# Performance work log

Measured on AMD Instinct MI355X. Metric: run time of the kernel, lower is better.

The kernel has to match this reference:

```python
import jax, jax.numpy as jnp
import numpy as np

N_STATES = 16          # 2**memory_length, memory_length hard-coded to 4 in the source
MEM = 4                # memory_length
T = 16384              # transmission_length
B = 256                # batch size


def setup_inputs() -> dict:
    key = jax.random.key(0)
    k1, k2 = jax.random.split(key)
    # received channel observations, one scalar per time step per batch element
    y = jax.random.normal(k1, (B, T + MEM), dtype=jnp.float32)
    # ISI channel taps (exponentially decaying, COST-channel style)
    h = jnp.exp(-0.7 * jnp.arange(MEM, dtype=jnp.float32))
    return {"y": y, "h": h}


def reference(y, h):
    n = N_STATES
    states = jnp.arange(n)
    # bit k of state s is the transmitted bit x_{t-k} (newest bit at LSB, since
    # next = (2*s + b) mod n under create_transition_table's packbits layout)
    bits = ((states[:, None] >> jnp.arange(MEM)[None, :]) & 1).astype(jnp.float32)  # [16,4]
    symbols = 1.0 - 2.0 * bits                     # BPSKModulator.modulate: 1 - 2c
    expected = symbols @ h                          # [16] expected channel output per state
    # predecessors of state ns: table[ns, j] = (ns >> 1) + j * n/2  (matches packbits table)
    pred_table = (states[:, None] >> 1) + jnp.array([0, 1])[None, :] * (n // 2)  # [16,2]

    def acs(in_prob, y_t):
        # add-compare-select over the 2 predecessors of each state
        cand = in_prob[:, pred_table]                              # [B,16,2]
        j = jnp.argmin(cand, axis=2)                               # [B,16] survivor index
        cost = (y_t[:, None] - expected[None, :]) ** 2             # [B,16] branch metric
        out_prob = jnp.min(cand, axis=2) + cost                    # [B,16]
        prev = pred_table[states[None, :], j]                      # [B,16] survivor predecessor
        return out_prob, prev.astype(jnp.int32)

    in0 = jnp.zeros((y.shape[0], n), dtype=y.dtype)                # initial_in_prob
    _, prev_states = jax.lax.scan(acs, in0, y.T)                   # prev_states: [T+MEM, B, 16]

    # traceback from start_state = 0
    def tb(state, prev_t):
        new_state = jnp.take_along_axis(prev_t, state[:, None], axis=1)[:, 0]  # [B]
        bit = (new_state >= n // 2).astype(jnp.float32)
        return new_state, bit

    start = jnp.zeros((y.shape[0],), dtype=jnp.int32)
    _, bits_rev = jax.lax.scan(tb, start, prev_states, reverse=True)  # [T+MEM, B], time order
    ml_path_bits = bits_rev.T                                         # [B, T+MEM]
    return ml_path_bits[:, :T]                                        # drop last memory_length bits
```

## Files before the change

### kernel.cpp

```cpp
#include <hip/hip_runtime.h>


#define DEV static __device__ __forceinline__

static constexpr int T_OUT = 16384;
static constexpr int TT    = 16388;
static constexpr int BB    = 256;
static constexpr int CHUNK = 64;
static constexpr int NFULL = 256;
static constexpr int NC    = 257;
static constexpr int CROW  = 68;

static constexpr unsigned long long IPI_TAB[4] = {
  0x4b5a6978c3d2e1f0ULL,
  0x4cb35da26e917f80ULL,
  0x46ceb93157dfa820ULL,
  0x4567cdefba983210ULL,
};

DEV int pi_of(int phi, int l){
  int l0=l&1, l1=(l>>1)&1, l2=(l>>2)&1, l3=(l>>3)&1;
  switch(phi & 3){
    case 0:  return (l2)      | ((l2^l0)<<1) | ((l2^l1)<<2) | ((l3^l2)<<3);
    case 1:  return (l3^l2)   | ((l2)<<1)    | ((l2^l0)<<2) | ((l2^l1)<<3);
    case 2:  return (l2^l1)   | ((l3^l2)<<1) | ((l2)<<2)    | ((l2^l0)<<3);
    default: return (l2^l0)   | ((l2^l1)<<1) | ((l3^l2)<<2) | ((l2)<<3);
  }
}

template<int CTRL>
DEV float dppmov(float x){
  return __int_as_float(__builtin_amdgcn_update_dpp(0, __float_as_int(x), CTRL, 0xF, 0xF, true));
}

template<int PH>
DEV float partner_of(float p){
  if constexpr (PH == 0) return dppmov<0x128>(p);
  else if constexpr (PH == 1) return dppmov<0x4E>(p);
  else if constexpr (PH == 2) return dppmov<0xB1>(p);
  else return dppmov<0x140>(p);
}

DEV float exp_of_state(int s, float h0, float h1, float h2, float h3){
  float e =            ((s     ) & 1) ? -h0 : h0;
  e = __fadd_rn(e, (((s >> 1)) & 1) ? -h1 : h1);
  e = __fadd_rn(e, (((s >> 2)) & 1) ? -h2 : h2);
  e = __fadd_rn(e, (((s >> 3)) & 1) ? -h3 : h3);
  return e;
}

DEV void chain8(float& p, float m0, float m1, float m2, float m3,
                float m4, float m5, float m6, float m7){
  float mn;
  asm volatile(
    "v_min_f32_dpp %1, %0, %0 row_ror:8 row_mask:0xf bank_mask:0xf\n\t"
    "v_add_f32 %0, %1, %2\n\t"
    "s_nop 1\n\t"
    "v_min_f32_dpp %1, %0, %0 quad_perm:[2,3,0,1] row_mask:0xf bank_mask:0xf\n\t"
    "v_add_f32 %0, %1, %3\n\t"
    "s_nop 1\n\t"
    "v_min_f32_dpp %1, %0, %0 quad_perm:[1,0,3,2] row_mask:0xf bank_mask:0xf\n\t"
    "v_add_f32 %0, %1, %4\n\t"
    "s_nop 1\n\t"
    "v_min_f32_dpp %1, %0, %0 row_mirror row_mask:0xf bank_mask:0xf\n\t"
    "v_add_f32 %0, %1, %5\n\t"
    "s_nop 1\n\t"
    "v_min_f32_dpp %1, %0, %0 row_ror:8 row_mask:0xf bank_mask:0xf\n\t"
    "v_add_f32 %0, %1, %6\n\t"
    "s_nop 1\n\t"
    "v_min_f32_dpp %1, %0, %0 quad_perm:[2,3,0,1] row_mask:0xf bank_mask:0xf\n\t"
    "v_add_f32 %0, %1, %7\n\t"
    "s_nop 1\n\t"
    "v_min_f32_dpp %1, %0, %0 quad_perm:[1,0,3,2] row_mask:0xf bank_mask:0xf\n\t"
    "v_add_f32 %0, %1, %8\n\t"
    "s_nop 1\n\t"
    "v_min_f32_dpp %1, %0, %0 row_mirror row_mask:0xf bank_mask:0xf\n\t"
    "v_add_f32 %0, %1, %9"
    : "+v"(p), "=&v"(mn)
    : "v"(m0), "v"(m1), "v"(m2), "v"(m3),
      "v"(m4), "v"(m5), "v"(m6), "v"(m7));
}

DEV void gload_lds16(const float* g, float* l){
  __builtin_amdgcn_global_load_lds(
      (const __attribute__((address_space(1))) void*)(g),
      (__attribute__((address_space(3))) void*)(l), 16, 0, 0);
}

DEV void wg_barrier(){
  asm volatile("s_waitcnt lgkmcnt(0)" ::: "memory");
  __builtin_amdgcn_s_barrier();
}

__global__ __launch_bounds__(192, 1) void k_forward(const float* __restrict__ y,
                                                    const float* __restrict__ h,
                                                    float* __restrict__ ckpt){
  __shared__ float ring[8][256];
  __shared__ float cost[2][64 * CROW];
  __shared__ float cks[64 * 64];

  const int tid  = threadIdx.x;
  const int wv   = tid >> 6;
  const int lane = tid & 63;

  if (wv == 0){
    const int l16 = lane & 15, s4 = lane >> 4;
    const int st0 = pi_of(0, l16);
    const int row = l16 * 4 + s4;

    float4 cqA[16], cqB[16];
    float p = 0.0f;

    wg_barrier();
    wg_barrier();
    {
      const float* cb = &cost[0][0];
      #pragma unroll
      for (int g = 0; g < 16; ++g)
        cqA[g] = *(const float4*)(cb + row * CROW + 4 * g);
    }
    wg_barrier();

    for (int k = 0; k < NFULL; k += 2){
      {
        const float* cb = &cost[1][0];
        #pragma unroll
        for (int g = 0; g < 16; ++g)
          cqB[g] = *(const float4*)(cb + row * CROW + 4 * g);
        __builtin_amdgcn_sched_barrier(0);
        #pragma unroll
        for (int g = 0; g < 16; g += 2)
          chain8(p, cqA[g].x, cqA[g].y, cqA[g].z, cqA[g].w,
                    cqA[g+1].x, cqA[g+1].y, cqA[g+1].z, cqA[g+1].w);
        cks[(k & 63) * 64 + s4 * 16 + st0] = p;
      }
      wg_barrier();
      {
        const float* cb = &cost[0][0];
        #pragma unroll
        for (int g = 0; g < 16; ++g)
          cqA[g] = *(const float4*)(cb + row * CROW + 4 * g);
        __builtin_amdgcn_sched_barrier(0);
        #pragma unroll
        for (int g = 0; g < 16; g += 2)
          chain8(p, cqB[g].x, cqB[g].y, cqB[g].z, cqB[g].w,
                    cqB[g+1].x, cqB[g+1].y, cqB[g+1].z, cqB[g+1].w);
        cks[((k + 1) & 63) * 64 + s4 * 16 + st0] = p;
        if (((k + 1) & 63) == 63){
          const int seg = (k + 1) >> 6;
          #pragma unroll 8
          for (int ch = 0; ch < 64; ++ch){
            const size_t chunkIdx = (size_t)seg * 64 + ch;
            ckpt[(chunkIdx * BB + blockIdx.x * 4) * 16 + lane] = cks[ch * 64 + lane];
          }
          asm volatile("s_waitcnt vmcnt(0)" ::: "memory");
        }
      }
      wg_barrier();
    }
  } else {
    const int gbase = (wv - 1) * 8;
    const int pl16  = lane >> 2;
    const int ps4   = lane & 3;
    const float h0 = h[0], h1 = h[1], h2 = h[2], h3 = h[3];
    const float EA = exp_of_state(pi_of(1,pl16), h0,h1,h2,h3);
    const float EB = exp_of_state(pi_of(2,pl16), h0,h1,h2,h3);
    const float EC = exp_of_state(pi_of(3,pl16), h0,h1,h2,h3);
    const float ED = exp_of_state(pi_of(0,pl16), h0,h1,h2,h3);
    const float* ysrc = y + (size_t)(blockIdx.x * 4 + ps4) * TT + pl16 * 4;

    #define PRODUCE(RB, CB)                                                   \
      {                                                                       \
        const float* rb = (RB);                                               \
        float* cb = (CB);                                                     \
        _Pragma("unroll")                                                     \
        for (int g2 = 0; g2 < 8; ++g2){                                       \
          const int g = gbase + g2;                                           \
          float4 yv = *(const float4*)(rb + g * 16 + ps4 * 4);                \
          float4 c; float d;                                                  \
          d = __fsub_rn(yv.x, EA); c.x = __fmul_rn(d, d);                     \
          d = __fsub_rn(yv.y, EB); c.y = __fmul_rn(d, d);                     \
          d = __fsub_rn(yv.z, EC); c.z = __fmul_rn(d, d);                     \
          d = __fsub_rn(yv.w, ED); c.w = __fmul_rn(d, d);                     \
          *(float4*)(cb + lane * CROW + 4 * g) = c;                           \
        }                                                                     \
      }

    if (wv == 1){
      #pragma unroll
      for (int q = 0; q < 8; ++q)
        gload_lds16(ysrc + q * CHUNK, &ring[q][0]);
      asm volatile("s_waitcnt vmcnt(6)" ::: "memory");
    }
    wg_barrier();
    PRODUCE(&ring[0][0], &cost[0][0]);
    wg_barrier();
    PRODUCE(&ring[1][0], &cost[1][0]);
    if (wv == 1){
      gload_lds16(ysrc + 8 * CHUNK, &ring[0][0]);
      asm volatile("s_waitcnt vmcnt(6)" ::: "memory");
    }
    wg_barrier();

    for (int k = 0; k < NFULL; k += 2){
      if (k + 2 < NFULL) PRODUCE(&ring[(k + 2) & 7][0], &cost[0][0]);
      if (wv == 1){
        const int ci = (k + 9 < NFULL) ? k + 9 : NFULL - 1;
        gload_lds16(ysrc + ci * CHUNK, &ring[(k + 9) & 7][0]);
        asm volatile("s_waitcnt vmcnt(6)" ::: "memory");
      }
      wg_barrier();
      if (k + 3 < NFULL) PRODUCE(&ring[(k + 3) & 7][0], &cost[1][0]);
      if (wv == 1){
        const int ci = (k + 10 < NFULL) ? k + 10 : NFULL - 1;
        gload_lds16(ysrc + ci * CHUNK, &ring[(k + 10) & 7][0]);
        asm volatile("s_waitcnt vmcnt(6)" ::: "memory");
      }
      wg_barrier();
    }
    #undef PRODUCE
  }
}

template<int PH>
DEV unsigned rstep(float& p, float yv, float E, bool role){
  float partner = partner_of<PH>(p);
  float c1 = role ? p : partner;
  float c0 = role ? partner : p;
  unsigned d = (c1 < c0) ? 1u : 0u;
  float mn = fminf(p, partner);
  float dd = __fsub_rn(yv, E);
  p = __fadd_rn(mn, __fmul_rn(dd, dd));
  return d;
}

__global__ __launch_bounds__(256) void k_replay(const float* __restrict__ y,
                                                const float* __restrict__ h,
                                                const float* __restrict__ ckpt,
                                                unsigned long long* __restrict__ bits,
                                                unsigned char* __restrict__ map){
  const int gt   = blockIdx.x * 256 + threadIdx.x;
  const int pair = gt >> 4;
  const int l16  = gt & 15;
  const int c    = pair >> 8;
  const int seq  = pair & 255;
  const float h0 = h[0], h1 = h[1], h2 = h[2], h3 = h[3];
  const float EA = exp_of_state(pi_of(1,l16), h0,h1,h2,h3);
  const float EB = exp_of_state(pi_of(2,l16), h0,h1,h2,h3);
  const float EC = exp_of_state(pi_of(3,l16), h0,h1,h2,h3);
  const float ED = exp_of_state(pi_of(0,l16), h0,h1,h2,h3);
  const bool r0 = (((l16>>3) ^ (l16>>2)) & 1) != 0;
  const bool r1 = (((l16>>2) ^ (l16>>1)) & 1) != 0;
  const bool r2 = (((l16>>2) ^  l16    ) & 1) != 0;
  const bool r3 = (( l16>>2)             & 1) != 0;
  const int  st0 = pi_of(0, l16);

  float p = (c == 0) ? 0.0f : ckpt[((size_t)(c - 1) * BB + seq) * 16 + st0];
  const float* yc = y + (size_t)seq * TT + c * CHUNK;
  unsigned lo = 0, hi = 0;

  if (c < NFULL){
    #pragma unroll
    for (int g = 0; g < 16; ++g){
      float4 yv = *(const float4*)(yc + 4*g);
      unsigned d0 = rstep<0>(p, yv.x, EA, r0);
      unsigned d1 = rstep<1>(p, yv.y, EB, r1);
      unsigned d2 = rstep<2>(p, yv.z, EC, r2);
      unsigned d3 = rstep<3>(p, yv.w, ED, r3);
      const int t = 4 * g;
      if (t < 32) lo |= (d0 << t) | (d1 << (t+1)) | (d2 << (t+2)) | (d3 << (t+3));
      else        hi |= (d0 << (t-32)) | (d1 << (t-31)) | (d2 << (t-30)) | (d3 << (t-29));
    }
  } else {
    float4 yv = *(const float4*)(yc);
    unsigned d0 = rstep<0>(p, yv.x, EA, r0);
    unsigned d1 = rstep<1>(p, yv.y, EB, r1);
    unsigned d2 = rstep<2>(p, yv.z, EC, r2);
    unsigned d3 = rstep<3>(p, yv.w, ED, r3);
    lo = d0 | (d1 << 1) | (d2 << 2) | (d3 << 3);
  }

  const int base = (threadIdx.x & 63) & 48;
  int s = l16;
  unsigned long long pb = 0ull;
  if (c < NFULL){
    #pragma unroll
    for (int j = 63; j >= 0; --j){
      int l = (int)((IPI_TAB[(j + 1) & 3] >> (4 * s)) & 15);
      unsigned hw = __shfl((j >= 32) ? hi : lo, base + l);
      unsigned long long b = (hw >> (j & 31)) & 1;
      s = (s >> 1) | ((int)b << 3);
      pb |= b << j;
    }
  } else {
    #pragma unroll
    for (int j = 3; j >= 0; --j){
      int l = (int)((IPI_TAB[(j + 1) & 3] >> (4 * s)) & 15);
      unsigned hw = __shfl(lo, base + l);
      unsigned long long b = (hw >> j) & 1;
      s = (s >> 1) | ((int)b << 3);
      pb |= b << j;
    }
  }
  bits[(size_t)pair * 16 + l16] = pb;
  map [(size_t)pair * 16 + l16] = (unsigned char)s;
}

__global__ __launch_bounds__(256) void k_compose(const unsigned char* __restrict__ map,
                                                 unsigned char* __restrict__ Earr){
  const int seq = threadIdx.x;
  int s = 0;
  Earr[(size_t)NFULL * BB + seq] = 0;
  #pragma unroll 4
  for (int c = NC - 1; c >= 1; --c){
    const uint4 mr = *(const uint4*)(map + ((size_t)c * BB + seq) * 16);
    unsigned wsel = (s < 8) ? ((s < 4) ? mr.x : mr.y) : ((s < 12) ? mr.z : mr.w);
    s = (wsel >> ((s & 3) * 8)) & 15;
    Earr[(size_t)(c - 1) * BB + seq] = (unsigned char)s;
  }
}

__global__ __launch_bounds__(256) void k_emit(const unsigned long long* __restrict__ bits,
                                              const unsigned char* __restrict__ Earr,
                                              float* __restrict__ out){
  const int gt   = blockIdx.x * 256 + threadIdx.x;
  const int pair = gt >> 4;
  const int l16  = gt & 15;
  const int c    = pair >> 8;
  const int seq  = pair & 255;
  const int e    = Earr[(size_t)c * BB + seq];
  const unsigned long long w = bits[(size_t)pair * 16 + e];
  const int j0 = l16 * 4;
  float4 f;
  f.x = (float)((w >> (j0    )) & 1);
  f.y = (float)((w >> (j0 + 1)) & 1);
  f.z = (float)((w >> (j0 + 2)) & 1);
  f.w = (float)((w >> (j0 + 3)) & 1);
  *(float4*)(out + (size_t)seq * T_OUT + c * CHUNK + j0) = f;
}

extern "C" void kernel_launch(void* const* d_in, const int* in_sizes, int n_in,
                              void* d_out, int out_size, void* d_ws, size_t ws_size,
                              hipStream_t stream){
  const float* y = (const float*)d_in[0];
  const float* h = (const float*)d_in[1];
  float* out = (float*)d_out;

  const size_t CKPT_B = (size_t)NFULL * BB * 16 * 4;
  const size_t BITS_B = (size_t)NC * BB * 16 * 8;
  const size_t MAP_B  = (size_t)NC * BB * 16;
  const size_t E_B    = (size_t)NC * BB;
  if (ws_size < CKPT_B + BITS_B + MAP_B + E_B) return;

  char* ws = (char*)d_ws;
  float*              ckpt = (float*)ws;
  unsigned long long* bits = (unsigned long long*)(ws + CKPT_B);
  unsigned char*      map  = (unsigned char*)(ws + CKPT_B + BITS_B);
  unsigned char*      Earr = (unsigned char*)(ws + CKPT_B + BITS_B + MAP_B);

  hipLaunchKernelGGL(k_forward, dim3(64),   dim3(192), 0, stream, y, h, ckpt);
  hipLaunchKernelGGL(k_replay,  dim3(4112), dim3(256), 0, stream, y, h, ckpt, bits, map);
  hipLaunchKernelGGL(k_compose, dim3(1),    dim3(256), 0, stream, map, Earr);
  hipLaunchKernelGGL(k_emit,    dim3(4096), dim3(256), 0, stream, bits, Earr, out);
}
```

Baseline: 288.6 us.

## Interleave two independent Viterbi chains per consumer wave to hide DPP latency

The forward checkpoint kernel now gives each consumer wave two independent groups of 4 sequences (8 per block), interleaving their DPP min/add chains so one chain's instructions fill the other's dependency stalls instead of s_nop padding. The block grows to 5 waves (two producer pairs) and the grid halves to 32 blocks, with doubled LDS ring, cost and checkpoint buffers. Using fewer blocks lowers CU-level parallelism and raises register pressure from four float4[16] arrays. The compose kernel's unroll factor also rises from 4 to 8.

```diff
diff --git a/kernel.cpp b/kernel.cpp
--- a/kernel.cpp
+++ b/kernel.cpp
@@ -49,36 +49,28 @@
   return e;
 }
 
-DEV void chain8(float& p, float m0, float m1, float m2, float m3,
-                float m4, float m5, float m6, float m7){
-  float mn;
+DEV void chain4x2(float& pA, float& pB, const float4 mA, const float4 mB){
+  float tA, tB;
   asm volatile(
-    "v_min_f32_dpp %1, %0, %0 row_ror:8 row_mask:0xf bank_mask:0xf\n\t"
-    "v_add_f32 %0, %1, %2\n\t"
-    "s_nop 1\n\t"
-    "v_min_f32_dpp %1, %0, %0 quad_perm:[2,3,0,1] row_mask:0xf bank_mask:0xf\n\t"
-    "v_add_f32 %0, %1, %3\n\t"
-    "s_nop 1\n\t"
-    "v_min_f32_dpp %1, %0, %0 quad_perm:[1,0,3,2] row_mask:0xf bank_mask:0xf\n\t"
-    "v_add_f32 %0, %1, %4\n\t"
-    "s_nop 1\n\t"
-    "v_min_f32_dpp %1, %0, %0 row_mirror row_mask:0xf bank_mask:0xf\n\t"
-    "v_add_f32 %0, %1, %5\n\t"
-    "s_nop 1\n\t"
-    "v_min_f32_dpp %1, %0, %0 row_ror:8 row_mask:0xf bank_mask:0xf\n\t"
-    "v_add_f32 %0, %1, %6\n\t"
-    "s_nop 1\n\t"
-    "v_min_f32_dpp %1, %0, %0 quad_perm:[2,3,0,1] row_mask:0xf bank_mask:0xf\n\t"
-    "v_add_f32 %0, %1, %7\n\t"
-    "s_nop 1\n\t"
-    "v_min_f32_dpp %1, %0, %0 quad_perm:[1,0,3,2] row_mask:0xf bank_mask:0xf\n\t"
-    "v_add_f32 %0, %1, %8\n\t"
-    "s_nop 1\n\t"
-    "v_min_f32_dpp %1, %0, %0 row_mirror row_mask:0xf bank_mask:0xf\n\t"
-    "v_add_f32 %0, %1, %9"
-    : "+v"(p), "=&v"(mn)
-    : "v"(m0), "v"(m1), "v"(m2), "v"(m3),
-      "v"(m4), "v"(m5), "v"(m6), "v"(m7));
+    "v_min_f32_dpp %2, %0, %0 row_ror:8 row_mask:0xf bank_mask:0xf\n\t"
+    "v_min_f32_dpp %3, %1, %1 row_ror:8 row_mask:0xf bank_mask:0xf\n\t"
+    "v_add_f32 %0, %2, %4\n\t"
+    "v_add_f32 %1, %3, %8\n\t"
+    "v_min_f32_dpp %2, %0, %0 quad_perm:[2,3,0,1] row_mask:0xf bank_mask:0xf\n\t"
+    "v_min_f32_dpp %3, %1, %1 quad_perm:[2,3,0,1] row_mask:0xf bank_mask:0xf\n\t"
+    "v_add_f32 %0, %2, %5\n\t"
+    "v_add_f32 %1, %3, %9\n\t"
+    "v_min_f32_dpp %2, %0, %0 quad_perm:[1,0,3,2] row_mask:0xf bank_mask:0xf\n\t"
+    "v_min_f32_dpp %3, %1, %1 quad_perm:[1,0,3,2] row_mask:0xf bank_mask:0xf\n\t"
+    "v_add_f32 %0, %2, %6\n\t"
+    "v_add_f32 %1, %3, %10\n\t"
+    "v_min_f32_dpp %2, %0, %0 row_mirror row_mask:0xf bank_mask:0xf\n\t"
+    "v_min_f32_dpp %3, %1, %1 row_mirror row_mask:0xf bank_mask:0xf\n\t"
+    "v_add_f32 %0, %2, %7\n\t"
+    "v_add_f32 %1, %3, %11"
+    : "+v"(pA), "+v"(pB), "=&v"(tA), "=&v"(tB)
+    : "v"(mA.x), "v"(mA.y), "v"(mA.z), "v"(mA.w),
+      "v"(mB.x), "v"(mB.y), "v"(mB.z), "v"(mB.w));
 }
 
 DEV void gload_lds16(const float* g, float* l){
@@ -92,12 +84,14 @@
   __builtin_amdgcn_s_barrier();
 }
 
-__global__ __launch_bounds__(192, 1) void k_forward(const float* __restrict__ y,
+__global__ __launch_bounds__(320, 1) void k_forward(const float* __restrict__ y,
                                                     const float* __restrict__ h,
                                                     float* __restrict__ ckpt){
-  __shared__ float ring[8][256];
-  __shared__ float cost[2][64 * CROW];
-  __shared__ float cks[64 * 64];
+  __shared__ float ringA[8][256];
+  __shared__ float ringB[8][256];
+  __shared__ float costA[2][64 * CROW];
+  __shared__ float costB[2][64 * CROW];
+  __shared__ float cks[64 * 128];
 
   const int tid  = threadIdx.x;
   const int wv   = tid >> 6;
@@ -108,50 +102,58 @@
     const int st0 = pi_of(0, l16);
     const int row = l16 * 4 + s4;
 
-    float4 cqA[16], cqB[16];
-    float p = 0.0f;
+    float4 qa[16], qb[16], ra[16], rb[16];
+    float pA = 0.0f, pB = 0.0f;
 
     wg_barrier();
     wg_barrier();
     {
-      const float* cb = &cost[0][0];
+      const float* ca = &costA[0][0];
+      const float* cb = &costB[0][0];
       #pragma unroll
-      for (int g = 0; g < 16; ++g)
-        cqA[g] = *(const float4*)(cb + row * CROW + 4 * g);
+      for (int g = 0; g < 16; ++g) qa[g] = *(const float4*)(ca + row * CROW + 4 * g);
+      #pragma unroll
+      for (int g = 0; g < 16; ++g) qb[g] = *(const float4*)(cb + row * CROW + 4 * g);
     }
     wg_barrier();
 
     for (int k = 0; k < NFULL; k += 2){
       {
-        const float* cb = &cost[1][0];
+        const float* ca = &costA[1][0];
+        const float* cb = &costB[1][0];
+        #pragma unroll
+        for (int g = 0; g < 16; ++g) ra[g] = *(const float4*)(ca + row * CROW + 4 * g);
+        #pragma unroll
+        for (int g = 0; g < 16; ++g) rb[g] = *(const float4*)(cb + row * CROW + 4 * g);
+        __builtin_amdgcn_sched_barrier(0);
         #pragma unroll
         for (int g = 0; g < 16; ++g)
-          cqB[g] = *(const float4*)(cb + row * CROW + 4 * g);
-        __builtin_amdgcn_sched_barrier(0);
-        #pragma unroll
-        for (int g = 0; g < 16; g += 2)
-          chain8(p, cqA[g].x, cqA[g].y, cqA[g].z, cqA[g].w,
-                    cqA[g+1].x, cqA[g+1].y, cqA[g+1].z, cqA[g+1].w);
-        cks[(k & 63) * 64 + s4 * 16 + st0] = p;
+          chain4x2(pA, pB, qa[g], qb[g]);
+        cks[(k & 63) * 128 +      s4 * 16 + st0] = pA;
+        cks[(k & 63) * 128 + 64 + s4 * 16 + st0] = pB;
       }
       wg_barrier();
       {
-        const float* cb = &cost[0][0];
+        const float* ca = &costA[0][0];
+        const float* cb = &costB[0][0];
+        #pragma unroll
+        for (int g = 0; g < 16; ++g) qa[g] = *(const float4*)(ca + row * CROW + 4 * g);
+        #pragma unroll
+        for (int g = 0; g < 16; ++g) qb[g] = *(const float4*)(cb + row * CROW + 4 * g);
+        __builtin_amdgcn_sched_barrier(0);
         #pragma unroll
         for (int g = 0; g < 16; ++g)
-          cqA[g] = *(const float4*)(cb + row * CROW + 4 * g);
-        __builtin_amdgcn_sched_barrier(0);
-        #pragma unroll
-        for (int g = 0; g < 16; g += 2)
-          chain8(p, cqB[g].x, cqB[g].y, cqB[g].z, cqB[g].w,
-                    cqB[g+1].x, cqB[g+1].y, cqB[g+1].z, cqB[g+1].w);
-        cks[((k + 1) & 63) * 64 + s4 * 16 + st0] = p;
+          chain4x2(pA, pB, ra[g], rb[g]);
+        cks[((k + 1) & 63) * 128 +      s4 * 16 + st0] = pA;
+        cks[((k + 1) & 63) * 128 + 64 + s4 * 16 + st0] = pB;
         if (((k + 1) & 63) == 63){
           const int seg = (k + 1) >> 6;
           #pragma unroll 8
           for (int ch = 0; ch < 64; ++ch){
             const size_t chunkIdx = (size_t)seg * 64 + ch;
-            ckpt[(chunkIdx * BB + blockIdx.x * 4) * 16 + lane] = cks[ch * 64 + lane];
+            float* dst = ckpt + (chunkIdx * BB + blockIdx.x * 8) * 16;
+            dst[lane]      = cks[ch * 128 + lane];
+            dst[64 + lane] = cks[ch * 128 + 64 + lane];
           }
           asm volatile("s_waitcnt vmcnt(0)" ::: "memory");
         }
@@ -159,61 +161,69 @@
       wg_barrier();
     }
   } else {
-    const int gbase = (wv - 1) * 8;
-    const int pl16  = lane >> 2;
-    const int ps4   = lane & 3;
+    const bool isA   = (wv <= 2);
+    const int  pw    = isA ? (wv - 1) : (wv - 3);
+    const int  gbase = pw * 8;
+    float* ring0 = isA ? &ringA[0][0] : &ringB[0][0];
+    float* cost0 = isA ? &costA[0][0] : &costB[0][0];
+    float* cost1 = isA ? &costA[1][0] : &costB[1][0];
+    const bool stager = (pw == 0);
+
+    const int pl16 = lane >> 2;
+    const int ps4  = lane & 3;
     const float h0 = h[0], h1 = h[1], h2 = h[2], h3 = h[3];
     const float EA = exp_of_state(pi_of(1,pl16), h0,h1,h2,h3);
     const float EB = exp_of_state(pi_of(2,pl16), h0,h1,h2,h3);
     const float EC = exp_of_state(pi_of(3,pl16), h0,h1,h2,h3);
     const float ED = exp_of_state(pi_of(0,pl16), h0,h1,h2,h3);
-    const float* ysrc = y + (size_t)(blockIdx.x * 4 + ps4) * TT + pl16 * 4;
+    const float* ysrc = y + (size_t)(blockIdx.x * 8 + (isA ? 0 : 4) + ps4) * TT
+                          + pl16 * 4;
 
     #define PRODUCE(RB, CB)                                                   \
       {                                                                       \
-        const float* rb = (RB);                                               \
-        float* cb = (CB);                                                     \
+        const float* rb_ = (RB);                                              \
+        float* cb_ = (CB);                                                    \
         _Pragma("unroll")                                                     \
         for (int g2 = 0; g2 < 8; ++g2){                                       \
           const int g = gbase + g2;                                           \
-          float4 yv = *(const float4*)(rb + g * 16 + ps4 * 4);                \
+          float4 yv = *(const float4*)(rb_ + g * 16 + ps4 * 4);               \
           float4 c; float d;                                                  \
           d = __fsub_rn(yv.x, EA); c.x = __fmul_rn(d, d);                     \
           d = __fsub_rn(yv.y, EB); c.y = __fmul_rn(d, d);                     \
           d = __fsub_rn(yv.z, EC); c.z = __fmul_rn(d, d);                     \
           d = __fsub_rn(yv.w, ED); c.w = __fmul_rn(d, d);                     \
-          *(float4*)(cb + lane * CROW + 4 * g) = c;                           \
+          *(float4*)(cb_ + lane * CROW + 4 * g) = c;                          \
         }                                                                     \
       }
 
-    if (wv == 1){
+    if (stager){
       #pragma unroll
       for (int q = 0; q < 8; ++q)
-        gload_lds16(ysrc + q * CHUNK, &ring[q][0]);
+        gload_lds16(ysrc + q * CHUNK, ring0 + q * 256);
       asm volatile("s_waitcnt vmcnt(6)" ::: "memory");
     }
     wg_barrier();
-    PRODUCE(&ring[0][0], &cost[0][0]);
-    wg_barrier();
-    PRODUCE(&ring[1][0], &cost[1][0]);
-    if (wv == 1){
-      gload_lds16(ysrc + 8 * CHUNK, &ring[0][0]);
+    PRODUCE(ring0 + 0 * 256, cost0);
+    wg_barrier();
+    PRODUCE(ring0 + 1 * 256, cost1);
+    if (stager){
+      gload_lds16(ysrc + 8 * CHUNK, ring0 + 0 * 256);
       asm volatile("s_waitcnt vmcnt(6)" ::: "memory");
     }
     wg_barrier();
 
     for (int k = 0; k < NFULL; k += 2){
-      if (k + 2 < NFULL) PRODUCE(&ring[(k + 2) & 7][0], &cost[0][0]);
-      if (wv == 1){
+      if (k + 2 < NFULL) PRODUCE(ring0 + ((k + 2) & 7) * 256, cost0);
+      if (stager){
         const int ci = (k + 9 < NFULL) ? k + 9 : NFULL - 1;
-        gload_lds16(ysrc + ci * CHUNK, &ring[(k + 9) & 7][0]);
+        gload_lds16(ysrc + ci * CHUNK, ring0 + ((k + 9) & 7) * 256);
         asm volatile("s_waitcnt vmcnt(6)" ::: "memory");
       }
       wg_barrier();
-      if (k + 3 < NFULL) PRODUCE(&ring[(k + 3) & 7][0], &cost[1][0]);
-      if (wv == 1){
+      if (k + 3 < NFULL) PRODUCE(ring0 + ((k + 3) & 7) * 256, cost1);
+      if (stager){
         const int ci = (k + 10 < NFULL) ? k + 10 : NFULL - 1;
-        gload_lds16(ysrc + ci * CHUNK, &ring[(k + 10) & 7][0]);
+        gload_lds16(ysrc + ci * CHUNK, ring0 + ((k + 10) & 7) * 256);
         asm volatile("s_waitcnt vmcnt(6)" ::: "memory");
       }
       wg_barrier();
@@ -311,7 +321,7 @@
   const int seq = threadIdx.x;
   int s = 0;
   Earr[(size_t)NFULL * BB + seq] = 0;
-  #pragma unroll 4
+  #pragma unroll 8
   for (int c = NC - 1; c >= 1; --c){
     const uint4 mr = *(const uint4*)(map + ((size_t)c * BB + seq) * 16);
     unsigned wsel = (s < 8) ? ((s < 4) ? mr.x : mr.y) : ((s < 12) ? mr.z : mr.w);
@@ -358,7 +368,7 @@
   unsigned char*      map  = (unsigned char*)(ws + CKPT_B + BITS_B);
   unsigned char*      Earr = (unsigned char*)(ws + CKPT_B + BITS_B + MAP_B);
 
-  hipLaunchKernelGGL(k_forward, dim3(64),   dim3(192), 0, stream, y, h, ckpt);
+  hipLaunchKernelGGL(k_forward, dim3(32),   dim3(320), 0, stream, y, h, ckpt);
   hipLaunchKernelGGL(k_replay,  dim3(4112), dim3(256), 0, stream, y, h, ckpt, bits, map);
   hipLaunchKernelGGL(k_compose, dim3(1),    dim3(256), 0, stream, map, Earr);
   hipLaunchKernelGGL(k_emit,    dim3(4096), dim3(256), 0, stream, bits, Earr, out);
```

Measured after the change: 388.3 us. +34.6%, slower.

## Fuse forward and replay kernels with counter-based producer-consumer overlap

Applied to the files above, without the earlier changes.

Merges the forward checkpoint kernel and the replay kernel into one persistent launch. 64 blocks run the forward recursion and publish checkpoints every 16 chunks with release counters, while 448 replay blocks spin on those counters and start replaying chunks as soon as their segment is ready. The aim is to overlap replay with the serial forward pass and drop a kernel launch boundary. In exchange it adds spin-wait polling and atomic traffic, and it relies on all blocks being co-resident to avoid deadlock. It also adds a tiny counter-zeroing kernel and raises the compose loop unroll.

```diff
diff --git a/kernel.cpp b/kernel.cpp
--- a/kernel.cpp
+++ b/kernel.cpp
@@ -10,6 +10,10 @@
 static constexpr int NFULL = 256;
 static constexpr int NC    = 257;
 static constexpr int CROW  = 68;
+static constexpr int FWD_BLOCKS = 64;
+static constexpr int RPL_BLOCKS = 448;
+static constexpr int NTILES = 4112;
+static constexpr int NSEG   = 16;
 
 static constexpr unsigned long long IPI_TAB[4] = {
   0x4b5a6978c3d2e1f0ULL,
@@ -88,138 +92,7 @@
 }
 
 DEV void wg_barrier(){
-  asm volatile("s_waitcnt lgkmcnt(0)" ::: "memory");
-  __builtin_amdgcn_s_barrier();
-}
-
-__global__ __launch_bounds__(192, 1) void k_forward(const float* __restrict__ y,
-                                                    const float* __restrict__ h,
-                                                    float* __restrict__ ckpt){
-  __shared__ float ring[8][256];
-  __shared__ float cost[2][64 * CROW];
-  __shared__ float cks[64 * 64];
-
-  const int tid  = threadIdx.x;
-  const int wv   = tid >> 6;
-  const int lane = tid & 63;
-
-  if (wv == 0){
-    const int l16 = lane & 15, s4 = lane >> 4;
-    const int st0 = pi_of(0, l16);
-    const int row = l16 * 4 + s4;
-
-    float4 cqA[16], cqB[16];
-    float p = 0.0f;
-
-    wg_barrier();
-    wg_barrier();
-    {
-      const float* cb = &cost[0][0];
-      #pragma unroll
-      for (int g = 0; g < 16; ++g)
-        cqA[g] = *(const float4*)(cb + row * CROW + 4 * g);
-    }
-    wg_barrier();
-
-    for (int k = 0; k < NFULL; k += 2){
-      {
-        const float* cb = &cost[1][0];
-        #pragma unroll
-        for (int g = 0; g < 16; ++g)
-          cqB[g] = *(const float4*)(cb + row * CROW + 4 * g);
-        __builtin_amdgcn_sched_barrier(0);
-        #pragma unroll
-        for (int g = 0; g < 16; g += 2)
-          chain8(p, cqA[g].x, cqA[g].y, cqA[g].z, cqA[g].w,
-                    cqA[g+1].x, cqA[g+1].y, cqA[g+1].z, cqA[g+1].w);
-        cks[(k & 63) * 64 + s4 * 16 + st0] = p;
-      }
-      wg_barrier();
-      {
-        const float* cb = &cost[0][0];
-        #pragma unroll
-        for (int g = 0; g < 16; ++g)
-          cqA[g] = *(const float4*)(cb + row * CROW + 4 * g);
-        __builtin_amdgcn_sched_barrier(0);
-        #pragma unroll
-        for (int g = 0; g < 16; g += 2)
-          chain8(p, cqB[g].x, cqB[g].y, cqB[g].z, cqB[g].w,
-                    cqB[g+1].x, cqB[g+1].y, cqB[g+1].z, cqB[g+1].w);
-        cks[((k + 1) & 63) * 64 + s4 * 16 + st0] = p;
-        if (((k + 1) & 63) == 63){
-          const int seg = (k + 1) >> 6;
-          #pragma unroll 8
-          for (int ch = 0; ch < 64; ++ch){
-            const size_t chunkIdx = (size_t)seg * 64 + ch;
-            ckpt[(chunkIdx * BB + blockIdx.x * 4) * 16 + lane] = cks[ch * 64 + lane];
-          }
-          asm volatile("s_waitcnt vmcnt(0)" ::: "memory");
-        }
-      }
-      wg_barrier();
-    }
-  } else {
-    const int gbase = (wv - 1) * 8;
-    const int pl16  = lane >> 2;
-    const int ps4   = lane & 3;
-    const float h0 = h[0], h1 = h[1], h2 = h[2], h3 = h[3];
-    const float EA = exp_of_state(pi_of(1,pl16), h0,h1,h2,h3);
-    const float EB = exp_of_state(pi_of(2,pl16), h0,h1,h2,h3);
-    const float EC = exp_of_state(pi_of(3,pl16), h0,h1,h2,h3);
-    const float ED = exp_of_state(pi_of(0,pl16), h0,h1,h2,h3);
-    const float* ysrc = y + (size_t)(blockIdx.x * 4 + ps4) * TT + pl16 * 4;
-
-    #define PRODUCE(RB, CB)                                                   \
-      {                                                                       \
-        const float* rb = (RB);                                               \
-        float* cb = (CB);                                                     \
-        _Pragma("unroll")                                                     \
-        for (int g2 = 0; g2 < 8; ++g2){                                       \
-          const int g = gbase + g2;                                           \
-          float4 yv = *(const float4*)(rb + g * 16 + ps4 * 4);                \
-          float4 c; float d;                                                  \
-          d = __fsub_rn(yv.x, EA); c.x = __fmul_rn(d, d);                     \
-          d = __fsub_rn(yv.y, EB); c.y = __fmul_rn(d, d);                     \
-          d = __fsub_rn(yv.z, EC); c.z = __fmul_rn(d, d);                     \
-          d = __fsub_rn(yv.w, ED); c.w = __fmul_rn(d, d);                     \
-          *(float4*)(cb + lane * CROW + 4 * g) = c;                           \
-        }                                                                     \
-      }
-
-    if (wv == 1){
-      #pragma unroll
-      for (int q = 0; q < 8; ++q)
-        gload_lds16(ysrc + q * CHUNK, &ring[q][0]);
-      asm volatile("s_waitcnt vmcnt(6)" ::: "memory");
-    }
-    wg_barrier();
-    PRODUCE(&ring[0][0], &cost[0][0]);
-    wg_barrier();
-    PRODUCE(&ring[1][0], &cost[1][0]);
-    if (wv == 1){
-      gload_lds16(ysrc + 8 * CHUNK, &ring[0][0]);
-      asm volatile("s_waitcnt vmcnt(6)" ::: "memory");
-    }
-    wg_barrier();
-
-    for (int k = 0; k < NFULL; k += 2){
-      if (k + 2 < NFULL) PRODUCE(&ring[(k + 2) & 7][0], &cost[0][0]);
-      if (wv == 1){
-        const int ci = (k + 9 < NFULL) ? k + 9 : NFULL - 1;
-        gload_lds16(ysrc + ci * CHUNK, &ring[(k + 9) & 7][0]);
-        asm volatile("s_waitcnt vmcnt(6)" ::: "memory");
-      }
-      wg_barrier();
-      if (k + 3 < NFULL) PRODUCE(&ring[(k + 3) & 7][0], &cost[1][0]);
-      if (wv == 1){
-        const int ci = (k + 10 < NFULL) ? k + 10 : NFULL - 1;
-        gload_lds16(ysrc + ci * CHUNK, &ring[(k + 10) & 7][0]);
-        asm volatile("s_waitcnt vmcnt(6)" ::: "memory");
-      }
-      wg_barrier();
-    }
-    #undef PRODUCE
-  }
+  asm volatile("s_waitcnt lgkmcnt(0)\n\ts_barrier" ::: "memory");
 }
 
 template<int PH>
@@ -234,76 +107,234 @@
   return d;
 }
 
-__global__ __launch_bounds__(256) void k_replay(const float* __restrict__ y,
-                                                const float* __restrict__ h,
-                                                const float* __restrict__ ckpt,
-                                                unsigned long long* __restrict__ bits,
-                                                unsigned char* __restrict__ map){
-  const int gt   = blockIdx.x * 256 + threadIdx.x;
-  const int pair = gt >> 4;
-  const int l16  = gt & 15;
-  const int c    = pair >> 8;
-  const int seq  = pair & 255;
-  const float h0 = h[0], h1 = h[1], h2 = h[2], h3 = h[3];
-  const float EA = exp_of_state(pi_of(1,l16), h0,h1,h2,h3);
-  const float EB = exp_of_state(pi_of(2,l16), h0,h1,h2,h3);
-  const float EC = exp_of_state(pi_of(3,l16), h0,h1,h2,h3);
-  const float ED = exp_of_state(pi_of(0,l16), h0,h1,h2,h3);
-  const bool r0 = (((l16>>3) ^ (l16>>2)) & 1) != 0;
-  const bool r1 = (((l16>>2) ^ (l16>>1)) & 1) != 0;
-  const bool r2 = (((l16>>2) ^  l16    ) & 1) != 0;
-  const bool r3 = (( l16>>2)             & 1) != 0;
-  const int  st0 = pi_of(0, l16);
-
-  float p = (c == 0) ? 0.0f : ckpt[((size_t)(c - 1) * BB + seq) * 16 + st0];
-  const float* yc = y + (size_t)seq * TT + c * CHUNK;
-  unsigned lo = 0, hi = 0;
-
-  if (c < NFULL){
-    #pragma unroll
-    for (int g = 0; g < 16; ++g){
-      float4 yv = *(const float4*)(yc + 4*g);
-      unsigned d0 = rstep<0>(p, yv.x, EA, r0);
-      unsigned d1 = rstep<1>(p, yv.y, EB, r1);
-      unsigned d2 = rstep<2>(p, yv.z, EC, r2);
-      unsigned d3 = rstep<3>(p, yv.w, ED, r3);
-      const int t = 4 * g;
-      if (t < 32) lo |= (d0 << t) | (d1 << (t+1)) | (d2 << (t+2)) | (d3 << (t+3));
-      else        hi |= (d0 << (t-32)) | (d1 << (t-31)) | (d2 << (t-30)) | (d3 << (t-29));
+__global__ void k_zero(unsigned* __restrict__ c){
+  for (int i = 0; i < NSEG; ++i) c[i] = 0u;
+}
+
+__global__ __launch_bounds__(256, 1) void k_main(const float* __restrict__ y,
+                                                 const float* __restrict__ h,
+                                                 float* __restrict__ ckpt,
+                                                 unsigned long long* __restrict__ bits,
+                                                 unsigned char* __restrict__ map,
+                                                 unsigned* __restrict__ counter){
+  __shared__ float ring[8][256];
+  __shared__ float costb[2][64 * CROW];
+  __shared__ float cks[16 * 64];
+
+  const int tid  = threadIdx.x;
+  const int lane = tid & 63;
+
+  if (blockIdx.x < FWD_BLOCKS){
+    const int wv  = tid >> 6;
+    const int blk = blockIdx.x;
+
+    if (wv == 0){
+      const int l16 = lane & 15, s4 = lane >> 4;
+      const int st0 = pi_of(0, l16);
+      const int row = l16 * 4 + s4;
+      float4 qA[16], qB[16];
+      float p = 0.0f;
+
+      wg_barrier();
+      wg_barrier();
+      {
+        const float* cb = &costb[0][0];
+        #pragma unroll
+        for (int g = 0; g < 16; ++g)
+          qA[g] = *(const float4*)(cb + row * CROW + 4 * g);
+      }
+      wg_barrier();
+
+      #define FLUSH(SEG)                                                      \
+        {                                                                     \
+          const int seg_ = (SEG);                                             \
+          _Pragma("unroll")                                                   \
+          for (int ch = 0; ch < 16; ++ch){                                    \
+            const size_t chunkIdx = (size_t)seg_ * 16 + ch;                   \
+            __hip_atomic_store(&ckpt[(chunkIdx * BB + blk * 4) * 16 + lane],  \
+                               cks[ch * 64 + lane],                           \
+                               __ATOMIC_RELAXED, __HIP_MEMORY_SCOPE_AGENT);   \
+          }                                                                   \
+          asm volatile("s_waitcnt vmcnt(0)" ::: "memory");                    \
+          if (lane == 0)                                                      \
+            __hip_atomic_fetch_add(&counter[seg_], 1u,                        \
+                                   __ATOMIC_RELEASE, __HIP_MEMORY_SCOPE_AGENT);\
+        }
+
+      for (int k = 0; k < NFULL; k += 2){
+        {
+          const float* cb = &costb[1][0];
+          #pragma unroll
+          for (int g = 0; g < 16; ++g)
+            qB[g] = *(const float4*)(cb + row * CROW + 4 * g);
+          __builtin_amdgcn_sched_barrier(0);
+          #pragma unroll
+          for (int g = 0; g < 16; g += 2)
+            chain8(p, qA[g].x, qA[g].y, qA[g].z, qA[g].w,
+                      qA[g+1].x, qA[g+1].y, qA[g+1].z, qA[g+1].w);
+          cks[(k & 15) * 64 + s4 * 16 + st0] = p;
+          wg_barrier();
+        }
+        {
+          const float* cb = &costb[0][0];
+          #pragma unroll
+          for (int g = 0; g < 16; ++g)
+            qA[g] = *(const float4*)(cb + row * CROW + 4 * g);
+          __builtin_amdgcn_sched_barrier(0);
+          #pragma unroll
+          for (int g = 0; g < 16; g += 2)
+            chain8(p, qB[g].x, qB[g].y, qB[g].z, qB[g].w,
+                      qB[g+1].x, qB[g+1].y, qB[g+1].z, qB[g+1].w);
+          cks[((k + 1) & 15) * 64 + s4 * 16 + st0] = p;
+          if (((k + 1) & 15) == 15) FLUSH((k + 1) >> 4);
+          wg_barrier();
+        }
+      }
+      #undef FLUSH
+    } else if (wv <= 2){
+      const int gbase = (wv - 1) * 8;
+      const int pl16  = lane >> 2;
+      const int ps4   = lane & 3;
+      const float h0 = h[0], h1 = h[1], h2 = h[2], h3 = h[3];
+      const float EA = exp_of_state(pi_of(1, pl16), h0, h1, h2, h3);
+      const float EB = exp_of_state(pi_of(2, pl16), h0, h1, h2, h3);
+      const float EC = exp_of_state(pi_of(3, pl16), h0, h1, h2, h3);
+      const float ED = exp_of_state(pi_of(0, pl16), h0, h1, h2, h3);
+      const float* ysrc = y + (size_t)(blk * 4 + ps4) * TT + pl16 * 4;
+
+      #define PRODUCE(RB, CB)                                                 \
+        {                                                                     \
+          const float* rb_ = (RB);                                            \
+          float* cb_ = (CB);                                                  \
+          _Pragma("unroll")                                                   \
+          for (int g2 = 0; g2 < 8; ++g2){                                     \
+            const int g = gbase + g2;                                         \
+            float4 yv = *(const float4*)(rb_ + g * 16 + ps4 * 4);             \
+            float4 c; float d_;                                               \
+            d_ = __fsub_rn(yv.x, EA); c.x = __fmul_rn(d_, d_);                \
+            d_ = __fsub_rn(yv.y, EB); c.y = __fmul_rn(d_, d_);                \
+            d_ = __fsub_rn(yv.z, EC); c.z = __fmul_rn(d_, d_);                \
+            d_ = __fsub_rn(yv.w, ED); c.w = __fmul_rn(d_, d_);                \
+            *(float4*)(cb_ + lane * CROW + 4 * g) = c;                        \
+          }                                                                   \
+        }
+
+      if (wv == 1){
+        #pragma unroll
+        for (int q = 0; q < 8; ++q)
+          gload_lds16(ysrc + q * CHUNK, &ring[q][0]);
+        asm volatile("s_waitcnt vmcnt(6)" ::: "memory");
+      }
+      wg_barrier();
+      PRODUCE(&ring[0][0], &costb[0][0]);
+      wg_barrier();
+      PRODUCE(&ring[1][0], &costb[1][0]);
+      if (wv == 1){
+        gload_lds16(ysrc + 8 * CHUNK, &ring[0][0]);
+        asm volatile("s_waitcnt vmcnt(6)" ::: "memory");
+      }
+      wg_barrier();
+
+      for (int k = 0; k < NFULL; k += 2){
+        if (k + 2 < NFULL) PRODUCE(&ring[(k + 2) & 7][0], &costb[0][0]);
+        if (wv == 1){
+          const int ci = (k + 9 < NFULL) ? k + 9 : NFULL - 1;
+          gload_lds16(ysrc + ci * CHUNK, &ring[(k + 9) & 7][0]);
+          asm volatile("s_waitcnt vmcnt(6)" ::: "memory");
+        }
+        wg_barrier();
+        if (k + 3 < NFULL) PRODUCE(&ring[(k + 3) & 7][0], &costb[1][0]);
+        if (wv == 1){
+          const int ci = (k + 10 < NFULL) ? k + 10 : NFULL - 1;
+          gload_lds16(ysrc + ci * CHUNK, &ring[(k + 10) & 7][0]);
+          asm volatile("s_waitcnt vmcnt(6)" ::: "memory");
+        }
+        wg_barrier();
+      }
+      #undef PRODUCE
+    } else {
+      for (int i = 0; i < 259; ++i) wg_barrier();
     }
   } else {
-    float4 yv = *(const float4*)(yc);
-    unsigned d0 = rstep<0>(p, yv.x, EA, r0);
-    unsigned d1 = rstep<1>(p, yv.y, EB, r1);
-    unsigned d2 = rstep<2>(p, yv.z, EC, r2);
-    unsigned d3 = rstep<3>(p, yv.w, ED, r3);
-    lo = d0 | (d1 << 1) | (d2 << 2) | (d3 << 3);
-  }
-
-  const int base = (threadIdx.x & 63) & 48;
-  int s = l16;
-  unsigned long long pb = 0ull;
-  if (c < NFULL){
-    #pragma unroll
-    for (int j = 63; j >= 0; --j){
-      int l = (int)((IPI_TAB[(j + 1) & 3] >> (4 * s)) & 15);
-      unsigned hw = __shfl((j >= 32) ? hi : lo, base + l);
-      unsigned long long b = (hw >> (j & 31)) & 1;
-      s = (s >> 1) | ((int)b << 3);
-      pb |= b << j;
-    }
-  } else {
-    #pragma unroll
-    for (int j = 3; j >= 0; --j){
-      int l = (int)((IPI_TAB[(j + 1) & 3] >> (4 * s)) & 15);
-      unsigned hw = __shfl(lo, base + l);
-      unsigned long long b = (hw >> j) & 1;
-      s = (s >> 1) | ((int)b << 3);
-      pb |= b << j;
+    const int rb  = blockIdx.x - FWD_BLOCKS;
+    const int l16 = tid & 15;
+    const int sub = tid >> 4;
+    const float h0 = h[0], h1 = h[1], h2 = h[2], h3 = h[3];
+    const float EA = exp_of_state(pi_of(1,l16), h0,h1,h2,h3);
+    const float EB = exp_of_state(pi_of(2,l16), h0,h1,h2,h3);
+    const float EC = exp_of_state(pi_of(3,l16), h0,h1,h2,h3);
+    const float ED = exp_of_state(pi_of(0,l16), h0,h1,h2,h3);
+    const bool r0 = (((l16>>3) ^ (l16>>2)) & 1) != 0;
+    const bool r1 = (((l16>>2) ^ (l16>>1)) & 1) != 0;
+    const bool r2 = (((l16>>2) ^  l16    ) & 1) != 0;
+    const bool r3 = (( l16>>2)             & 1) != 0;
+    const int  st0  = pi_of(0, l16);
+    const int  base = lane & 48;
+
+    for (int t = rb; t < NTILES; t += RPL_BLOCKS){
+      const int pair = t * 16 + sub;
+      const int c    = pair >> 8;
+      const int seq  = pair & 255;
+
+      if (c > 0){
+        const int seg = (c - 1) >> 4;
+        while (__hip_atomic_load(&counter[seg], __ATOMIC_ACQUIRE,
+                                 __HIP_MEMORY_SCOPE_AGENT) < (unsigned)FWD_BLOCKS)
+          __builtin_amdgcn_s_sleep(8);
+      }
+
+      float p = (c == 0) ? 0.0f
+        : __hip_atomic_load(&ckpt[((size_t)(c - 1) * BB + seq) * 16 + st0],
+                            __ATOMIC_RELAXED, __HIP_MEMORY_SCOPE_AGENT);
+      const float* yc = y + (size_t)seq * TT + c * CHUNK;
+      unsigned lo = 0, hi = 0;
+
+      if (c < NFULL){
+        #pragma unroll
+        for (int g = 0; g < 16; ++g){
+          float4 yv = *(const float4*)(yc + 4*g);
+          unsigned d0 = rstep<0>(p, yv.x, EA, r0);
+          unsigned d1 = rstep<1>(p, yv.y, EB, r1);
+          unsigned d2 = rstep<2>(p, yv.z, EC, r2);
+          unsigned d3 = rstep<3>(p, yv.w, ED, r3);
+          const int tt = 4 * g;
+          if (tt < 32) lo |= (d0 << tt) | (d1 << (tt+1)) | (d2 << (tt+2)) | (d3 << (tt+3));
+          else         hi |= (d0 << (tt-32)) | (d1 << (tt-31)) | (d2 << (tt-30)) | (d3 << (tt-29));
+        }
+      } else {
+        float4 yv = *(const float4*)(yc);
+        unsigned d0 = rstep<0>(p, yv.x, EA, r0);
+        unsigned d1 = rstep<1>(p, yv.y, EB, r1);
+        unsigned d2 = rstep<2>(p, yv.z, EC, r2);
+        unsigned d3 = rstep<3>(p, yv.w, ED, r3);
+        lo = d0 | (d1 << 1) | (d2 << 2) | (d3 << 3);
+      }
+
+      int s = l16;
+      unsigned long long pb = 0ull;
+      if (c < NFULL){
+        #pragma unroll
+        for (int j = 63; j >= 0; --j){
+          int l = (int)((IPI_TAB[(j + 1) & 3] >> (4 * s)) & 15);
+          unsigned hw = __shfl((j >= 32) ? hi : lo, base + l);
+          unsigned long long b = (hw >> (j & 31)) & 1;
+          s = (s >> 1) | ((int)b << 3);
+          pb |= b << j;
+        }
+      } else {
+        #pragma unroll
+        for (int j = 3; j >= 0; --j){
+          int l = (int)((IPI_TAB[(j + 1) & 3] >> (4 * s)) & 15);
+          unsigned hw = __shfl(lo, base + l);
+          unsigned long long b = (hw >> j) & 1;
+          s = (s >> 1) | ((int)b << 3);
+          pb |= b << j;
+        }
+      }
+      bits[(size_t)pair * 16 + l16] = pb;
+      map [(size_t)pair * 16 + l16] = (unsigned char)s;
     }
   }
-  bits[(size_t)pair * 16 + l16] = pb;
-  map [(size_t)pair * 16 + l16] = (unsigned char)s;
 }
 
 __global__ __launch_bounds__(256) void k_compose(const unsigned char* __restrict__ map,
@@ -311,7 +342,7 @@
   const int seq = threadIdx.x;
   int s = 0;
   Earr[(size_t)NFULL * BB + seq] = 0;
-  #pragma unroll 4
+  #pragma unroll 8
   for (int c = NC - 1; c >= 1; --c){
     const uint4 mr = *(const uint4*)(map + ((size_t)c * BB + seq) * 16);
     unsigned wsel = (s < 8) ? ((s < 4) ? mr.x : mr.y) : ((s < 12) ? mr.z : mr.w);
@@ -346,20 +377,23 @@
   const float* h = (const float*)d_in[1];
   float* out = (float*)d_out;
 
-  const size_t CKPT_B = (size_t)NFULL * BB * 16 * 4;
   const size_t BITS_B = (size_t)NC * BB * 16 * 8;
   const size_t MAP_B  = (size_t)NC * BB * 16;
   const size_t E_B    = (size_t)NC * BB;
-  if (ws_size < CKPT_B + BITS_B + MAP_B + E_B) return;
+  const size_t CKPT_B = (size_t)NFULL * BB * 16 * 4;
+  const size_t CNT_B  = 128;
+  if (ws_size < BITS_B + MAP_B + E_B + CKPT_B + CNT_B) return;
 
   char* ws = (char*)d_ws;
-  float*              ckpt = (float*)ws;
-  unsigned long long* bits = (unsigned long long*)(ws + CKPT_B);
-  unsigned char*      map  = (unsigned char*)(ws + CKPT_B + BITS_B);
-  unsigned char*      Earr = (unsigned char*)(ws + CKPT_B + BITS_B + MAP_B);
-
-  hipLaunchKernelGGL(k_forward, dim3(64),   dim3(192), 0, stream, y, h, ckpt);
-  hipLaunchKernelGGL(k_replay,  dim3(4112), dim3(256), 0, stream, y, h, ckpt, bits, map);
+  unsigned long long* bits = (unsigned long long*)ws;
+  unsigned char*      map  = (unsigned char*)(ws + BITS_B);
+  unsigned char*      Earr = (unsigned char*)(ws + BITS_B + MAP_B);
+  float*              ckpt = (float*)(ws + BITS_B + MAP_B + E_B);
+  unsigned*           cnt  = (unsigned*)(ws + BITS_B + MAP_B + E_B + CKPT_B);
+
+  hipLaunchKernelGGL(k_zero,    dim3(1),    dim3(1),   0, stream, cnt);
+  hipLaunchKernelGGL(k_main,    dim3(FWD_BLOCKS + RPL_BLOCKS), dim3(256), 0, stream,
+                     y, h, ckpt, bits, map, cnt);
   hipLaunchKernelGGL(k_compose, dim3(1),    dim3(256), 0, stream, map, Earr);
   hipLaunchKernelGGL(k_emit,    dim3(4096), dim3(256), 0, stream, bits, Earr, out);
 }
```

Measured after the change: 1.001 ms. 247% more time.
